# Optimization experiments

Measured on AMD Instinct MI355X. Metric: run time of the kernel, lower is better.

The kernel has to match this reference:

```python
import math
import jax, jax.numpy as jnp
import numpy as np

HEAD = 16
DIM = 1024
DH = DIM // HEAD
NEG = -100000000.0


def setup_inputs() -> dict:
    key = jax.random.key(0)
    ks = jax.random.split(key, 12)
    B, S, D = 2, 2048, DIM
    s = 1.0 / math.sqrt(D)
    return {
        "key": jax.random.normal(ks[0], (B, S, D), jnp.float32),
        "value": jax.random.normal(ks[1], (B, S, D), jnp.float32),
        "query": jax.random.normal(ks[2], (B, S, D), jnp.float32),
        "mask": jax.random.randint(ks[3], (B, 1, S, S), 0, 2) == 1,
        "Wq": jax.random.normal(ks[4], (D, D), jnp.float32) * s,
        "bq": jnp.zeros((D,), jnp.float32),
        "Wk": jax.random.normal(ks[5], (D, D), jnp.float32) * s,
        "bk": jnp.zeros((D,), jnp.float32),
        "Wv": jax.random.normal(ks[6], (D, D), jnp.float32) * s,
        "bv": jnp.zeros((D,), jnp.float32),
        "Wo": jax.random.normal(ks[7], (D, D), jnp.float32) * s,
        "bo": jnp.zeros((D,), jnp.float32),
    }


def _split_heads(x, b):
    # [B, S, D] -> [B, H, S, Dh]
    return x.reshape(b, -1, HEAD, DH).transpose(0, 2, 1, 3)


def reference(key, value, query, mask, Wq, bq, Wk, bk, Wv, bv, Wo, bo):
    b, k_len, d = key.shape
    q_len = query.shape[1]
    k_up = _split_heads(key @ Wk.T + bk, b)
    v_up = _split_heads(value @ Wv.T + bv, b)
    q_up = _split_heads(query @ Wq.T + bq, b) / math.sqrt(DH)
    scores = jnp.einsum("bhqd,bhkd->bhqk", q_up, k_up)
    scores = jnp.where(mask, NEG, scores)
    attn = jax.nn.softmax(scores, axis=-1)
    # dropout is identity in eval/reference mode
    context = jnp.einsum("bhqk,bhkd->bhqd", attn, v_up)
    context = context.transpose(0, 2, 1, 3).reshape(b, q_len, d)
    out = context @ Wo.T + bo
    return out, attn
```

## Files before the change

### kernel.cpp

```cpp
#include <hip/hip_runtime.h>
#include <stdint.h>

#define S_LEN 2048
#define D_MODEL 1024
#define N_HEAD 16
#define D_HEAD 64
#define N_BATCH 2
#define M_TOK (N_BATCH * S_LEN)

typedef unsigned short u16;
typedef unsigned int u32;
typedef __attribute__((ext_vector_type(8))) short bf16x8;
typedef __attribute__((ext_vector_type(4))) short s16x4;
typedef __attribute__((ext_vector_type(4))) float f32x4;
typedef __attribute__((ext_vector_type(4))) unsigned short u16x4;

#define MFMA16(a, b, c) __builtin_amdgcn_mfma_f32_16x16x32_bf16((a), (b), (c), 0, 0, 0)

#if defined(__has_builtin)
#if __has_builtin(__builtin_amdgcn_mfma_f32_16x16x16bf16_1k)
#define HAVE_MFMA_16x16x16 1
#define MFMA_PV(a, b, c) __builtin_amdgcn_mfma_f32_16x16x16bf16_1k((a), (b), (c), 0, 0, 0)
#endif
#endif

#define WAITCNT(n) asm volatile("s_waitcnt vmcnt(" #n ")" ::: "memory")
#define BAR() __builtin_amdgcn_s_barrier()

__device__ __forceinline__ u16 f2bf(float f) {
  unsigned int u = __float_as_uint(f);
  u = (u + 0x7FFFu + ((u >> 16) & 1u)) >> 16;
  return (u16)u;
}

__device__ __forceinline__ void gload_lds16(const u16* g, u16* l) {
  __builtin_amdgcn_global_load_lds((const __attribute__((address_space(1))) void*)g,
                                   (__attribute__((address_space(3))) void*)l, 16, 0, 0);
}

#define N4BIG (M_TOK * D_MODEL / 4)
#define N4W (D_MODEL * D_MODEL / 4)
__global__ __launch_bounds__(256) void cvt7_kernel(
    const float* __restrict__ sk, const float* __restrict__ sv, const float* __restrict__ sq,
    const float* __restrict__ swq, const float* __restrict__ swk, const float* __restrict__ swv,
    const float* __restrict__ swo, u16* __restrict__ dk, u16* __restrict__ dv, u16* __restrict__ dq,
    u16* __restrict__ dwq, u16* __restrict__ dwk, u16* __restrict__ dwv, u16* __restrict__ dwo) {
  const float* s;
  u16* d;
  int n4;
  switch (blockIdx.y) {
    case 0: s = sk; d = dk; n4 = N4BIG; break;
    case 1: s = sv; d = dv; n4 = N4BIG; break;
    case 2: s = sq; d = dq; n4 = N4BIG; break;
    case 3: s = swq; d = dwq; n4 = N4W; break;
    case 4: s = swk; d = dwk; n4 = N4W; break;
    case 5: s = swv; d = dwv; n4 = N4W; break;
    default: s = swo; d = dwo; n4 = N4W; break;
  }
  int i = blockIdx.x * blockDim.x + threadIdx.x;
  int stride = gridDim.x * blockDim.x;
  for (; i < n4; i += stride) {
    float4 v = ((const float4*)s)[i];
    u16x4 o = {f2bf(v.x), f2bf(v.y), f2bf(v.z), f2bf(v.w)};
    ((u16x4*)d)[i] = o;
  }
}

__global__ __launch_bounds__(256) void pack_mask(const int* __restrict__ mask,
                                                 unsigned long long* __restrict__ packed) {
  int wid = (blockIdx.x * blockDim.x + threadIdx.x) >> 6;
  int lane = threadIdx.x & 63;
  int nw = (gridDim.x * blockDim.x) >> 6;
  const int NW64 = M_TOK * (S_LEN / 64);
  for (int widx = wid; widx < NW64; widx += nw) {
    int m = mask[(size_t)widx * 64 + lane];
    unsigned long long bits = __ballot(m != 0);
    if (lane == 0) packed[widx] = bits;
  }
}

__device__ __forceinline__ void gemm_body(const u16* __restrict__ A, const u16* __restrict__ Bw,
                                          const float* __restrict__ bias, void* __restrict__ Cout,
                                          float scale, int outmode) {
  __shared__ u16 As[128 * 32];
  __shared__ u16 Bs[128 * 32];
  const int K = D_MODEL, N = D_MODEL;
  int tid = threadIdx.x;
  int w = tid >> 6, lane = tid & 63, lg = lane >> 4, lr = lane & 15;
  int m0 = blockIdx.x * 128, n0 = blockIdx.y * 128;
  int wr = w >> 1, wc = w & 1;
  f32x4 acc[4][4] = {};
  int r0 = tid >> 2;
  int r1 = 64 + (tid >> 2);
  int kk0 = (tid & 3) * 8;
  for (int kb = 0; kb < K; kb += 32) {
    gload_lds16(A + (size_t)(m0 + r0) * K + kb + kk0, As + w * 512);
    gload_lds16(A + (size_t)(m0 + r1) * K + kb + kk0, As + 2048 + w * 512);
    gload_lds16(Bw + (size_t)(n0 + r0) * K + kb + kk0, Bs + w * 512);
    gload_lds16(Bw + (size_t)(n0 + r1) * K + kb + kk0, Bs + 2048 + w * 512);
    __syncthreads();
    bf16x8 af[4], bfr[4];
#pragma unroll
    for (int i = 0; i < 4; i++)
      af[i] = *(const bf16x8*)(As + (wr * 64 + i * 16 + lr) * 32 + lg * 8);
#pragma unroll
    for (int i = 0; i < 4; i++)
      bfr[i] = *(const bf16x8*)(Bs + (wc * 64 + i * 16 + lr) * 32 + lg * 8);
#pragma unroll
    for (int mi = 0; mi < 4; mi++)
#pragma unroll
      for (int ni = 0; ni < 4; ni++)
        acc[mi][ni] = MFMA16(af[mi], bfr[ni], acc[mi][ni]);
    __syncthreads();
  }
#pragma unroll
  for (int mi = 0; mi < 4; mi++)
#pragma unroll
    for (int ni = 0; ni < 4; ni++) {
      int col = n0 + wc * 64 + ni * 16 + lr;
      float bv = bias[col];
      if (outmode == 2) {
        int row0 = m0 + wr * 64 + mi * 16 + lg * 4;
        int bb = row0 >> 11, ss = row0 & (S_LEN - 1);
        u16x4 pk;
#pragma unroll
        for (int r = 0; r < 4; r++) pk[r] = f2bf((acc[mi][ni][r] + bv) * scale);
        *(u16x4*)((u16*)Cout + ((size_t)((bb * N_HEAD + (col >> 6)) * D_HEAD + (col & 63)) * S_LEN + ss)) = pk;
      } else {
#pragma unroll
        for (int r = 0; r < 4; r++) {
          int row = m0 + wr * 64 + mi * 16 + lg * 4 + r;
          float v = (acc[mi][ni][r] + bv) * scale;
          if (outmode == 1)
            ((float*)Cout)[(size_t)row * N + col] = v;
          else
            ((u16*)Cout)[(size_t)row * N + col] = f2bf(v);
        }
      }
    }
}

#define QSCALE 0.18033688011112042f

__global__ __launch_bounds__(256) void proj3_kernel(
    const u16* __restrict__ kbf, const u16* __restrict__ vbf, const u16* __restrict__ qbf,
    const u16* __restrict__ wkb, const u16* __restrict__ wvb, const u16* __restrict__ wqb,
    const float* __restrict__ bk, const float* __restrict__ bv, const float* __restrict__ bq,
    u16* __restrict__ kup, u16* __restrict__ vtg, u16* __restrict__ qup) {
  int z = blockIdx.z;
  if (z == 0)
    gemm_body(kbf, wkb, bk, kup, 1.0f, 0);
  else if (z == 1)
    gemm_body(vbf, wvb, bv, vtg, 1.0f, 2);
  else
    gemm_body(qbf, wqb, bq, qup, QSCALE, 0);
}

__global__ __launch_bounds__(256) void gemm_out_kernel(const u16* __restrict__ A,
                                                       const u16* __restrict__ Bw,
                                                       const float* __restrict__ bias,
                                                       float* __restrict__ C) {
  gemm_body(A, Bw, bias, C, 1.0f, 1);
}

__global__ __launch_bounds__(512, 4) void attn_kernel(
    const u16* __restrict__ Qup, const u16* __restrict__ Kup, const u16* __restrict__ Vt,
    const u32* __restrict__ mpack, float* __restrict__ attn_out, u16* __restrict__ ctx) {
  __shared__ u16 kbuf[2][128 * 64];
  __shared__ u16 vbuf[2][64 * 128];
#if !defined(HAVE_MFMA_16x16x16)
  __shared__ u16 pbuf[8][16 * 64];
#endif
  int tid = threadIdx.x;
  int w = tid >> 6, lane = tid & 63, lg = lane >> 4, lr = lane & 15;

  int fb = blockIdx.x;
  int logical = (fb & 7) * 64 + (fb >> 3);
  int qx = logical & 15;
  int h = (logical >> 4) & 15;
  int b = logical >> 8;
  int q0 = qx * 128;
  int q = q0 + w * 16 + lr;
  const float NEGV = -100000000.0f;

  bf16x8 qf0, qf1;
  {
    const u16* qrow = Qup + (size_t)(b * S_LEN + q) * D_MODEL + h * D_HEAD;
    qf0 = *(const bf16x8*)(qrow + lg * 8);
    qf1 = *(const bf16x8*)(qrow + 32 + lg * 8);
  }
  const u16* Kb = Kup + (size_t)(b * S_LEN) * D_MODEL + h * D_HEAD;
  const u16* Vb = Vt + (size_t)(b * N_HEAD + h) * D_HEAD * S_LEN;
  const u32* mrow = mpack + (size_t)(b * S_LEN + q) * (S_LEN / 32);
  float* attn_b = attn_out + ((size_t)(b * N_HEAD + h) * S_LEN + q) * S_LEN;

  int krow = tid >> 3;
  int kchunk = (tid & 7) ^ (krow & 7);
  const u16* KgA = Kb + (size_t)krow * D_MODEL + kchunk * 8;
  int vrow = tid >> 4;
  int vchunk = (tid & 15) ^ (vrow & 7);
  const u16* VgA = Vb + (size_t)vrow * S_LEN + vchunk * 8;
  const int sw = lr & 7;

#define STAGE_K(bn, ktn)                                                    \
  do {                                                                      \
    const u16* _s = KgA + (size_t)(ktn) * 128 * D_MODEL;                    \
    gload_lds16(_s, &kbuf[bn][0] + w * 512);                                \
    gload_lds16(_s + (size_t)64 * D_MODEL, &kbuf[bn][4096] + w * 512);      \
  } while (0)
#define STAGE_V(bn, ktn)                                                    \
  do {                                                                      \
    const u16* _s = VgA + (size_t)(ktn) * 128;                              \
    gload_lds16(_s, &vbuf[bn][0] + w * 512);                                \
    gload_lds16(_s + (size_t)32 * S_LEN, &vbuf[bn][4096] + w * 512);        \
  } while (0)

  float lsA = 0.f, lsB = 0.f;

#define P0_BODY(BN, MM)                                                     \
  {                                                                         \
    const u16* kc = &kbuf[BN][0];                                           \
    _Pragma("unroll") for (int t = 0; t < 8; t++) {                         \
      const u16* kr = kc + (t * 16 + lr) * 64;                              \
      bf16x8 k0 = *(const bf16x8*)(kr + ((lg ^ sw) << 3));                  \
      bf16x8 k1 = *(const bf16x8*)(kr + (((lg + 4) ^ sw) << 3));            \
      f32x4 a = {0.f, 0.f, 0.f, 0.f};                                       \
      a = MFMA16(k0, qf0, a);                                               \
      a = MFMA16(k1, qf1, a);                                               \
      u32 wbits = (t >> 1) == 0 ? (MM).x                                    \
                : (t >> 1) == 1 ? (MM).y                                    \
                : (t >> 1) == 2 ? (MM).z : (MM).w;                          \
      _Pragma("unroll") for (int r = 0; r < 4; r++) {                       \
        int j = (t * 16 + lg * 4 + r) & 31;                                 \
        float s = ((wbits >> j) & 1u) ? NEGV : a[r];                        \
        if (r & 1) lsB += exp2f(s); else lsA += exp2f(s);                   \
      }                                                                     \
    }                                                                       \
  }

  uint4 mA, mB;
  mA = *(const uint4*)(mrow);
  STAGE_K(0, 0);
  for (int it = 0; it < 7; it++) {
    int kt = it * 2;
    mB = *(const uint4*)(mrow + (kt + 1) * 4);
    STAGE_K(1, kt + 1);
    WAITCNT(3);
    BAR();
    P0_BODY(0, mA);
    BAR();
    mA = *(const uint4*)(mrow + (kt + 2) * 4);
    STAGE_K(0, kt + 2);
    WAITCNT(3);
    BAR();
    P0_BODY(1, mB);
    BAR();
  }
  mB = *(const uint4*)(mrow + 15 * 4);
  STAGE_K(1, 15);
  WAITCNT(3);
  BAR();
  P0_BODY(0, mA);
  BAR();
  WAITCNT(0);
  BAR();
  P0_BODY(1, mB);

  float lsum = lsA + lsB;
  lsum += __shfl_xor(lsum, 16);
  lsum += __shfl_xor(lsum, 32);
  float il2 = lsum > 0.f ? -__log2f(lsum) : 0.f;

  BAR();

  f32x4 ctxacc[4] = {};

#if defined(HAVE_MFMA_16x16x16)
#define P1_BODY(BN, MM, KT)                                                 \
  {                                                                         \
    const u16* kc = &kbuf[BN][0];                                           \
    const u16* vc = &vbuf[BN][0];                                           \
    _Pragma("unroll") for (int t = 0; t < 8; t++) {                         \
      const u16* kr = kc + (t * 16 + lr) * 64;                              \
      bf16x8 k0 = *(const bf16x8*)(kr + ((lg ^ sw) << 3));                  \
      bf16x8 k1 = *(const bf16x8*)(kr + (((lg + 4) ^ sw) << 3));            \
      f32x4 a = {0.f, 0.f, 0.f, 0.f};                                       \
      a = MFMA16(k0, qf0, a);                                                \
      a = MFMA16(k1, qf1, a);                                                \
      u32 wbits = (t >> 1) == 0 ? (MM).x                                    \
                : (t >> 1) == 1 ? (MM).y                                    \
                : (t >> 1) == 2 ? (MM).z : (MM).w;                          \
      f32x4 p;                                                              \
      u16x4 pb;                                                             \
      _Pragma("unroll") for (int r = 0; r < 4; r++) {                       \
        int j = (t * 16 + lg * 4 + r) & 31;                                 \
        float s = ((wbits >> j) & 1u) ? NEGV : (a[r] + il2);                \
        float pv = exp2f(s);                                                \
        p[r] = pv;                                                          \
        pb[r] = f2bf(pv);                                                   \
      }                                                                     \
      *(f32x4*)(attn_b + (KT) * 128 + t * 16 + lg * 4) = p;                 \
      s16x4 ap = {(short)pb[0], (short)pb[1], (short)pb[2], (short)pb[3]};  \
      _Pragma("unroll") for (int d = 0; d < 4; d++) {                       \
        s16x4 vf = *(const s16x4*)(vc + (d * 16 + lr) * 128 +               \
                                   (((t * 2 + (lg >> 1)) ^ sw) << 3) +      \
                                   ((lg & 1) << 2));                        \
        ctxacc[d] = MFMA_PV(ap, vf, ctxacc[d]);                             \
      }                                                                     \
    }                                                                       \
  }
#else
#define P1_BODY(BN, MM, KT)                                                 \
  {                                                                         \
    const u16* kc = &kbuf[BN][0];                                           \
    const u16* vc = &vbuf[BN][0];                                           \
    u16* pw = &pbuf[w][0];                                                  \
    _Pragma("unroll") for (int h2 = 0; h2 < 2; h2++) {                      \
      _Pragma("unroll") for (int tt = 0; tt < 4; tt++) {                    \
        const int t = h2 * 4 + tt;                                          \
        const u16* kr = kc + (t * 16 + lr) * 64;                            \
        bf16x8 k0 = *(const bf16x8*)(kr + ((lg ^ sw) << 3));                \
        bf16x8 k1 = *(const bf16x8*)(kr + (((lg + 4) ^ sw) << 3));          \
        f32x4 a = {0.f, 0.f, 0.f, 0.f};                                     \
        a = MFMA16(k0, qf0, a);                                              \
        a = MFMA16(k1, qf1, a);                                              \
        u32 wbits = (t >> 1) == 0 ? (MM).x                                  \
                  : (t >> 1) == 1 ? (MM).y                                  \
                  : (t >> 1) == 2 ? (MM).z : (MM).w;                        \
        f32x4 p;                                                            \
        u16x4 pb;                                                           \
        _Pragma("unroll") for (int r = 0; r < 4; r++) {                     \
          int j = (t * 16 + lg * 4 + r) & 31;                               \
          float s = ((wbits >> j) & 1u) ? NEGV : (a[r] + il2);              \
          float pv = exp2f(s);                                              \
          p[r] = pv;                                                        \
          pb[r] = f2bf(pv);                                                 \
        }                                                                   \
        *(f32x4*)(attn_b + (KT) * 128 + t * 16 + lg * 4) = p;               \
        *(u16x4*)(pw + lr * 64 + (((tt * 2 + (lg >> 1)) ^ sw) << 3) +       \
                  ((lg & 1) << 2)) = pb;                                    \
      }                                                                     \
      bf16x8 pa0 = *(const bf16x8*)(pw + lr * 64 + ((lg ^ sw) << 3));       \
      bf16x8 pa1 = *(const bf16x8*)(pw + lr * 64 + (((lg + 4) ^ sw) << 3)); \
      _Pragma("unroll") for (int d = 0; d < 4; d++) {                       \
        const u16* vr = vc + (d * 16 + lr) * 128 + (h2 << 6);               \
        bf16x8 v0 = *(const bf16x8*)(vr + ((lg ^ sw) << 3));                \
        bf16x8 v1 = *(const bf16x8*)(vr + (((lg + 4) ^ sw) << 3));          \
        ctxacc[d] = MFMA16(pa0, v0, ctxacc[d]);                             \
        ctxacc[d] = MFMA16(pa1, v1, ctxacc[d]);                             \
      }                                                                     \
    }                                                                       \
  }
#endif

  mA = *(const uint4*)(mrow);
  STAGE_K(0, 0);
  STAGE_V(0, 0);
  for (int it = 0; it < 7; it++) {
    int kt = it * 2;
    mB = *(const uint4*)(mrow + (kt + 1) * 4);
    STAGE_K(1, kt + 1);
    STAGE_V(1, kt + 1);
    WAITCNT(5);
    BAR();
    P1_BODY(0, mA, kt);
    BAR();
    mA = *(const uint4*)(mrow + (kt + 2) * 4);
    STAGE_K(0, kt + 2);
    STAGE_V(0, kt + 2);
    WAITCNT(5);
    BAR();
    P1_BODY(1, mB, kt + 1);
    BAR();
  }
  mB = *(const uint4*)(mrow + 15 * 4);
  STAGE_K(1, 15);
  STAGE_V(1, 15);
  WAITCNT(5);
  BAR();
  P1_BODY(0, mA, 14);
  BAR();
  WAITCNT(8);
  BAR();
  P1_BODY(1, mB, 15);

#pragma unroll
  for (int d = 0; d < 4; d++)
#pragma unroll
    for (int r = 0; r < 4; r++) {
      int sq = q0 + w * 16 + lg * 4 + r;
      ctx[(size_t)(b * S_LEN + sq) * D_MODEL + h * D_HEAD + d * 16 + lr] = f2bf(ctxacc[d][r]);
    }
#undef STAGE_K
#undef STAGE_V
#undef P0_BODY
#undef P1_BODY
}

#define O_KBF 0u
#define O_VBF 4194304u
#define O_QBF 8388608u
#define O_WQ 12582912u
#define O_WK 13631488u
#define O_WV 14680064u
#define O_WO 15728640u
#define O_QUP 16777216u
#define O_KUP 20971520u
#define O_VUP 25165824u
#define O_CTX 29360128u

extern "C" void kernel_launch(void* const* d_in, const int* in_sizes, int n_in,
                              void* d_out, int out_size, void* d_ws, size_t ws_size,
                              hipStream_t stream) {
  const float* key = (const float*)d_in[0];
  const float* value = (const float*)d_in[1];
  const float* query = (const float*)d_in[2];
  const int* mask = (const int*)d_in[3];
  const float* Wq = (const float*)d_in[4];
  const float* bq = (const float*)d_in[5];
  const float* Wk = (const float*)d_in[6];
  const float* bk = (const float*)d_in[7];
  const float* Wv = (const float*)d_in[8];
  const float* bv = (const float*)d_in[9];
  const float* Wo = (const float*)d_in[10];
  const float* bo = (const float*)d_in[11];

  u16* ws = (u16*)d_ws;
  u16* kbf = ws + O_KBF;
  u16* vbf = ws + O_VBF;
  u16* qbf = ws + O_QBF;
  u16* wqb = ws + O_WQ;
  u16* wkb = ws + O_WK;
  u16* wvb = ws + O_WV;
  u16* wob = ws + O_WO;
  u16* qup = ws + O_QUP;
  u16* kup = ws + O_KUP;
  u16* vtg = ws + O_VUP;
  u16* ctxb = ws + O_CTX;

  float* out = (float*)d_out;
  float* attn = out + (size_t)N_BATCH * S_LEN * D_MODEL;

  cvt7_kernel<<<dim3(512, 7), 256, 0, stream>>>(key, value, query, Wq, Wk, Wv, Wo, kbf, vbf, qbf,
                                                wqb, wkb, wvb, wob);
  proj3_kernel<<<dim3(32, 8, 3), 256, 0, stream>>>(kbf, vbf, qbf, wkb, wvb, wqb, bk, bv, bq, kup,
                                                   vtg, qup);
  pack_mask<<<1024, 256, 0, stream>>>(mask, (unsigned long long*)kbf);
  attn_kernel<<<512, 512, 0, stream>>>(qup, kup, vtg, (const u32*)kbf, attn, ctxb);
  gemm_out_kernel<<<dim3(32, 8), 256, 0, stream>>>(ctxb, wob, bo, out);
}
```

Baseline: 330.6 us.

## Load V fragments straight from global and use a 4-deep K LDS ring

The V tile is no longer staged through shared memory. Each wave reads its V operand fragments directly from global memory inside the PV loop. The LDS freed by dropping V is used for a 4-buffer ring of K tiles, staged two tiles ahead, which removes one barrier per tile in both passes. This cuts LDS traffic and synchronisation, but the direct V reads are small 8-byte, strided global loads that may add latency and waste bandwidth unless they hit cache.

```diff
diff --git a/kernel.cpp b/kernel.cpp
--- a/kernel.cpp
+++ b/kernel.cpp
@@ -166,8 +166,7 @@
 __global__ __launch_bounds__(512, 4) void attn_kernel(
     const u16* __restrict__ Qup, const u16* __restrict__ Kup, const u16* __restrict__ Vt,
     const u32* __restrict__ mpack, float* __restrict__ attn_out, u16* __restrict__ ctx) {
-  __shared__ u16 kbuf[2][128 * 64];
-  __shared__ u16 vbuf[2][64 * 128];
+  __shared__ u16 kbuf[4][128 * 64];
 #if !defined(HAVE_MFMA_16x16x16)
   __shared__ u16 pbuf[8][16 * 64];
 #endif
@@ -197,9 +196,6 @@
   int krow = tid >> 3;
   int kchunk = (tid & 7) ^ (krow & 7);
   const u16* KgA = Kb + (size_t)krow * D_MODEL + kchunk * 8;
-  int vrow = tid >> 4;
-  int vchunk = (tid & 15) ^ (vrow & 7);
-  const u16* VgA = Vb + (size_t)vrow * S_LEN + vchunk * 8;
   const int sw = lr & 7;
 
 #define STAGE_K(bn, ktn)                                                    \
@@ -207,12 +203,6 @@
     const u16* _s = KgA + (size_t)(ktn) * 128 * D_MODEL;                    \
     gload_lds16(_s, &kbuf[bn][0] + w * 512);                                \
     gload_lds16(_s + (size_t)64 * D_MODEL, &kbuf[bn][4096] + w * 512);      \
-  } while (0)
-#define STAGE_V(bn, ktn)                                                    \
-  do {                                                                      \
-    const u16* _s = VgA + (size_t)(ktn) * 128;                              \
-    gload_lds16(_s, &vbuf[bn][0] + w * 512);                                \
-    gload_lds16(_s + (size_t)32 * S_LEN, &vbuf[bn][4096] + w * 512);        \
   } while (0)
 
   float lsA = 0.f, lsB = 0.f;
@@ -241,30 +231,27 @@
   uint4 mA, mB;
   mA = *(const uint4*)(mrow);
   STAGE_K(0, 0);
+  STAGE_K(1, 1);
   for (int it = 0; it < 7; it++) {
     int kt = it * 2;
     mB = *(const uint4*)(mrow + (kt + 1) * 4);
-    STAGE_K(1, kt + 1);
-    WAITCNT(3);
+    STAGE_K((kt + 2) & 3, kt + 2);
+    WAITCNT(5);
     BAR();
-    P0_BODY(0, mA);
+    P0_BODY(kt & 3, mA);
+    mA = *(const uint4*)(mrow + (kt + 2) * 4);
+    STAGE_K((kt + 3) & 3, kt + 3);
+    WAITCNT(5);
     BAR();
-    mA = *(const uint4*)(mrow + (kt + 2) * 4);
-    STAGE_K(0, kt + 2);
-    WAITCNT(3);
-    BAR();
-    P0_BODY(1, mB);
-    BAR();
+    P0_BODY((kt + 1) & 3, mB);
   }
   mB = *(const uint4*)(mrow + 15 * 4);
-  STAGE_K(1, 15);
   WAITCNT(3);
   BAR();
-  P0_BODY(0, mA);
-  BAR();
+  P0_BODY(2, mA);
   WAITCNT(0);
   BAR();
-  P0_BODY(1, mB);
+  P0_BODY(3, mB);
 
   float lsum = lsA + lsB;
   lsum += __shfl_xor(lsum, 16);
@@ -279,14 +266,18 @@
 #define P1_BODY(BN, MM, KT)                                                 \
   {                                                                         \
     const u16* kc = &kbuf[BN][0];                                           \
-    const u16* vc = &vbuf[BN][0];                                           \
+    const u16* vg = Vb + (size_t)(KT) * 128;                                \
     _Pragma("unroll") for (int t = 0; t < 8; t++) {                         \
+      s16x4 vf0 = *(const s16x4*)(vg + (size_t)(0 * 16 + lr) * S_LEN + t * 16 + lg * 4); \
+      s16x4 vf1 = *(const s16x4*)(vg + (size_t)(1 * 16 + lr) * S_LEN + t * 16 + lg * 4); \
+      s16x4 vf2 = *(const s16x4*)(vg + (size_t)(2 * 16 + lr) * S_LEN + t * 16 + lg * 4); \
+      s16x4 vf3 = *(const s16x4*)(vg + (size_t)(3 * 16 + lr) * S_LEN + t * 16 + lg * 4); \
       const u16* kr = kc + (t * 16 + lr) * 64;                              \
       bf16x8 k0 = *(const bf16x8*)(kr + ((lg ^ sw) << 3));                  \
       bf16x8 k1 = *(const bf16x8*)(kr + (((lg + 4) ^ sw) << 3));            \
       f32x4 a = {0.f, 0.f, 0.f, 0.f};                                       \
-      a = MFMA16(k0, qf0, a);                                                \
-      a = MFMA16(k1, qf1, a);                                                \
+      a = MFMA16(k0, qf0, a);                                               \
+      a = MFMA16(k1, qf1, a);                                               \
       u32 wbits = (t >> 1) == 0 ? (MM).x                                    \
                 : (t >> 1) == 1 ? (MM).y                                    \
                 : (t >> 1) == 2 ? (MM).z : (MM).w;                          \
@@ -301,19 +292,17 @@
       }                                                                     \
       *(f32x4*)(attn_b + (KT) * 128 + t * 16 + lg * 4) = p;                 \
       s16x4 ap = {(short)pb[0], (short)pb[1], (short)pb[2], (short)pb[3]};  \
-      _Pragma("unroll") for (int d = 0; d < 4; d++) {                       \
-        s16x4 vf = *(const s16x4*)(vc + (d * 16 + lr) * 128 +               \
-                                   (((t * 2 + (lg >> 1)) ^ sw) << 3) +      \
-                                   ((lg & 1) << 2));                        \
-        ctxacc[d] = MFMA_PV(ap, vf, ctxacc[d]);                             \
-      }                                                                     \
+      ctxacc[0] = MFMA_PV(ap, vf0, ctxacc[0]);                              \
+      ctxacc[1] = MFMA_PV(ap, vf1, ctxacc[1]);                              \
+      ctxacc[2] = MFMA_PV(ap, vf2, ctxacc[2]);                              \
+      ctxacc[3] = MFMA_PV(ap, vf3, ctxacc[3]);                              \
     }                                                                       \
   }
 #else
 #define P1_BODY(BN, MM, KT)                                                 \
   {                                                                         \
     const u16* kc = &kbuf[BN][0];                                           \
-    const u16* vc = &vbuf[BN][0];                                           \
+    const u16* vg = Vb + (size_t)(KT) * 128;                                \
     u16* pw = &pbuf[w][0];                                                  \
     _Pragma("unroll") for (int h2 = 0; h2 < 2; h2++) {                      \
       _Pragma("unroll") for (int tt = 0; tt < 4; tt++) {                    \
@@ -343,9 +332,9 @@
       bf16x8 pa0 = *(const bf16x8*)(pw + lr * 64 + ((lg ^ sw) << 3));       \
       bf16x8 pa1 = *(const bf16x8*)(pw + lr * 64 + (((lg + 4) ^ sw) << 3)); \
       _Pragma("unroll") for (int d = 0; d < 4; d++) {                       \
-        const u16* vr = vc + (d * 16 + lr) * 128 + (h2 << 6);               \
-        bf16x8 v0 = *(const bf16x8*)(vr + ((lg ^ sw) << 3));                \
-        bf16x8 v1 = *(const bf16x8*)(vr + (((lg + 4) ^ sw) << 3));          \
+        const u16* vr = vg + (size_t)(d * 16 + lr) * S_LEN + h2 * 64;       \
+        bf16x8 v0 = *(const bf16x8*)(vr + lg * 8);                          \
+        bf16x8 v1 = *(const bf16x8*)(vr + 32 + lg * 8);                     \
         ctxacc[d] = MFMA16(pa0, v0, ctxacc[d]);                             \
         ctxacc[d] = MFMA16(pa1, v1, ctxacc[d]);                             \
       }                                                                     \
@@ -355,34 +344,27 @@
 
   mA = *(const uint4*)(mrow);
   STAGE_K(0, 0);
-  STAGE_V(0, 0);
+  STAGE_K(1, 1);
   for (int it = 0; it < 7; it++) {
     int kt = it * 2;
     mB = *(const uint4*)(mrow + (kt + 1) * 4);
-    STAGE_K(1, kt + 1);
-    STAGE_V(1, kt + 1);
+    STAGE_K((kt + 2) & 3, kt + 2);
     WAITCNT(5);
     BAR();
-    P1_BODY(0, mA, kt);
-    BAR();
+    P1_BODY(kt & 3, mA, kt);
     mA = *(const uint4*)(mrow + (kt + 2) * 4);
-    STAGE_K(0, kt + 2);
-    STAGE_V(0, kt + 2);
+    STAGE_K((kt + 3) & 3, kt + 3);
     WAITCNT(5);
     BAR();
-    P1_BODY(1, mB, kt + 1);
-    BAR();
+    P1_BODY((kt + 1) & 3, mB, kt + 1);
   }
   mB = *(const uint4*)(mrow + 15 * 4);
-  STAGE_K(1, 15);
-  STAGE_V(1, 15);
-  WAITCNT(5);
+  WAITCNT(3);
   BAR();
-  P1_BODY(0, mA, 14);
+  P1_BODY(2, mA, 14);
+  WAITCNT(0);
   BAR();
-  WAITCNT(8);
-  BAR();
-  P1_BODY(1, mB, 15);
+  P1_BODY(3, mB, 15);
 
 #pragma unroll
   for (int d = 0; d < 4; d++)
@@ -392,7 +374,6 @@
       ctx[(size_t)(b * S_LEN + sq) * D_MODEL + h * D_HEAD + d * 16 + lr] = f2bf(ctxacc[d][r]);
     }
 #undef STAGE_K
-#undef STAGE_V
 #undef P0_BODY
 #undef P1_BODY
 }
```

After: 468.7 us. 1.42x slower.

## Split attention into separate row-sum and probability/PV kernels with LDS-staged attn writes

Applied to the files above, without the earlier changes.

Splits the two-pass attention kernel into two launches. The first computes softmax row sums over half of the keys per block, using 2048 smaller blocks for more parallelism, and writes partial sums to workspace. The second kernel reads the two partial sums, uses 64-key tiles instead of 128, and stages each wave's fp32 probabilities through padded LDS so the attn matrix is written as coalesced row segments. The cost is an extra launch, extra K reads and mask reads in the first pass, more LDS use, and more barrier iterations.

```diff
diff --git a/kernel.cpp b/kernel.cpp
--- a/kernel.cpp
+++ b/kernel.cpp
@@ -163,17 +163,109 @@
   gemm_body(A, Bw, bias, C, 1.0f, 1);
 }
 
-__global__ __launch_bounds__(512, 4) void attn_kernel(
-    const u16* __restrict__ Qup, const u16* __restrict__ Kup, const u16* __restrict__ Vt,
-    const u32* __restrict__ mpack, float* __restrict__ attn_out, u16* __restrict__ ctx) {
-  __shared__ u16 kbuf[2][128 * 64];
-  __shared__ u16 vbuf[2][64 * 128];
-#if !defined(HAVE_MFMA_16x16x16)
-  __shared__ u16 pbuf[8][16 * 64];
-#endif
+__global__ __launch_bounds__(256, 8) void attn_p0(const u16* __restrict__ Qup,
+                                                  const u16* __restrict__ Kup,
+                                                  const u32* __restrict__ mpack,
+                                                  float* __restrict__ lsums) {
+  __shared__ u16 kbuf[2][64 * 64];
   int tid = threadIdx.x;
   int w = tid >> 6, lane = tid & 63, lg = lane >> 4, lr = lane & 15;
-
+  int fb = blockIdx.x;
+  int logical = (fb & 7) * 256 + (fb >> 3);
+  int khalf = logical & 1;
+  int qb = (logical >> 1) & 31;
+  int h = (logical >> 6) & 15;
+  int b = logical >> 10;
+  int q0 = qb * 64;
+  int q = q0 + w * 16 + lr;
+  const float NEGV = -100000000.0f;
+
+  bf16x8 qf0, qf1;
+  {
+    const u16* qrow = Qup + (size_t)(b * S_LEN + q) * D_MODEL + h * D_HEAD;
+    qf0 = *(const bf16x8*)(qrow + lg * 8);
+    qf1 = *(const bf16x8*)(qrow + 32 + lg * 8);
+  }
+  const u16* Kb = Kup + (size_t)(b * S_LEN) * D_MODEL + h * D_HEAD;
+  const u32* mrow = mpack + (size_t)(b * S_LEN + q) * (S_LEN / 32) + khalf * 32;
+
+  int srow = tid >> 3;
+  int schunk = (tid & 7) ^ (srow & 7);
+  const u16* KgA = Kb + (size_t)(khalf * 1024 + srow) * D_MODEL + schunk * 8;
+  const int sw = lr & 7;
+
+#define STAGE_K0(bn, ktn)                                                   \
+  do {                                                                      \
+    const u16* _s = KgA + (size_t)(ktn) * 64 * D_MODEL;                     \
+    gload_lds16(_s, &kbuf[bn][0] + w * 512);                                \
+    gload_lds16(_s + (size_t)32 * D_MODEL, &kbuf[bn][2048] + w * 512);      \
+  } while (0)
+
+  float lsA = 0.f, lsB = 0.f;
+#define P0_BODY(BN, MM)                                                     \
+  {                                                                         \
+    const u16* kc = &kbuf[BN][0];                                           \
+    _Pragma("unroll") for (int t = 0; t < 4; t++) {                         \
+      const u16* kr = kc + (t * 16 + lr) * 64;                              \
+      bf16x8 k0 = *(const bf16x8*)(kr + ((lg ^ sw) << 3));                  \
+      bf16x8 k1 = *(const bf16x8*)(kr + (((lg + 4) ^ sw) << 3));            \
+      f32x4 a = {0.f, 0.f, 0.f, 0.f};                                       \
+      a = MFMA16(k0, qf0, a);                                               \
+      a = MFMA16(k1, qf1, a);                                               \
+      u32 wbits = (t < 2) ? (MM).x : (MM).y;                                \
+      _Pragma("unroll") for (int r = 0; r < 4; r++) {                       \
+        int j = (t * 16 + lg * 4 + r) & 31;                                 \
+        float s = ((wbits >> j) & 1u) ? NEGV : a[r];                        \
+        if (r & 1) lsB += exp2f(s); else lsA += exp2f(s);                   \
+      }                                                                     \
+    }                                                                       \
+  }
+
+  uint2 mA, mB;
+  mA = *(const uint2*)(mrow);
+  STAGE_K0(0, 0);
+  for (int it = 0; it < 7; it++) {
+    int kt = it * 2;
+    mB = *(const uint2*)(mrow + (kt + 1) * 2);
+    STAGE_K0(1, kt + 1);
+    WAITCNT(3);
+    BAR();
+    P0_BODY(0, mA);
+    BAR();
+    mA = *(const uint2*)(mrow + (kt + 2) * 2);
+    STAGE_K0(0, kt + 2);
+    WAITCNT(3);
+    BAR();
+    P0_BODY(1, mB);
+    BAR();
+  }
+  mB = *(const uint2*)(mrow + 15 * 2);
+  STAGE_K0(1, 15);
+  WAITCNT(3);
+  BAR();
+  P0_BODY(0, mA);
+  BAR();
+  WAITCNT(0);
+  BAR();
+  P0_BODY(1, mB);
+
+  float lsum = lsA + lsB;
+  lsum += __shfl_xor(lsum, 16);
+  lsum += __shfl_xor(lsum, 32);
+  if (lg == 0) lsums[(size_t)khalf * 65536 + (size_t)(b * N_HEAD + h) * S_LEN + q] = lsum;
+#undef STAGE_K0
+#undef P0_BODY
+}
+
+__global__ __launch_bounds__(512, 4) void attn_p1(
+    const u16* __restrict__ Qup, const u16* __restrict__ Kup, const u16* __restrict__ Vt,
+    const u32* __restrict__ mpack, const float* __restrict__ lsums,
+    float* __restrict__ attn_out, u16* __restrict__ ctx) {
+  __shared__ u16 kbuf[2][64 * 64];
+  __shared__ u16 vbuf[2][64 * 64];
+  __shared__ float pbuf[8][16][68];
+  int tid = threadIdx.x;
+  int w = tid >> 6, lane = tid & 63, lg = lane >> 4, lr = lane & 15;
   int fb = blockIdx.x;
   int logical = (fb & 7) * 64 + (fb >> 3);
   int qx = logical & 15;
@@ -192,104 +284,54 @@
   const u16* Kb = Kup + (size_t)(b * S_LEN) * D_MODEL + h * D_HEAD;
   const u16* Vb = Vt + (size_t)(b * N_HEAD + h) * D_HEAD * S_LEN;
   const u32* mrow = mpack + (size_t)(b * S_LEN + q) * (S_LEN / 32);
-  float* attn_b = attn_out + ((size_t)(b * N_HEAD + h) * S_LEN + q) * S_LEN;
-
-  int krow = tid >> 3;
-  int kchunk = (tid & 7) ^ (krow & 7);
-  const u16* KgA = Kb + (size_t)krow * D_MODEL + kchunk * 8;
-  int vrow = tid >> 4;
-  int vchunk = (tid & 15) ^ (vrow & 7);
-  const u16* VgA = Vb + (size_t)vrow * S_LEN + vchunk * 8;
+  float* attn_w = attn_out + ((size_t)(b * N_HEAD + h) * S_LEN + q0 + w * 16) * S_LEN;
+
+  float il2;
+  {
+    size_t idx = (size_t)(b * N_HEAD + h) * S_LEN + q;
+    float tot = lsums[idx] + lsums[65536 + idx];
+    il2 = tot > 0.f ? -__log2f(tot) : 0.f;
+  }
+
+  int srow = tid >> 3;
+  int schunk = (tid & 7) ^ (srow & 7);
+  const u16* KgA = Kb + (size_t)srow * D_MODEL + schunk * 8;
+  const u16* VgA = Vb + (size_t)srow * S_LEN + schunk * 8;
   const int sw = lr & 7;
 
-#define STAGE_K(bn, ktn)                                                    \
-  do {                                                                      \
-    const u16* _s = KgA + (size_t)(ktn) * 128 * D_MODEL;                    \
-    gload_lds16(_s, &kbuf[bn][0] + w * 512);                                \
-    gload_lds16(_s + (size_t)64 * D_MODEL, &kbuf[bn][4096] + w * 512);      \
-  } while (0)
-#define STAGE_V(bn, ktn)                                                    \
-  do {                                                                      \
-    const u16* _s = VgA + (size_t)(ktn) * 128;                              \
-    gload_lds16(_s, &vbuf[bn][0] + w * 512);                                \
-    gload_lds16(_s + (size_t)32 * S_LEN, &vbuf[bn][4096] + w * 512);        \
-  } while (0)
-
-  float lsA = 0.f, lsB = 0.f;
-
-#define P0_BODY(BN, MM)                                                     \
+#define SK(bn, ktn) gload_lds16(KgA + (size_t)(ktn) * 64 * D_MODEL, &kbuf[bn][w * 512])
+#define SV(bn, ktn) gload_lds16(VgA + (size_t)(ktn) * 64, &vbuf[bn][w * 512])
+
+  f32x4 ctxacc[4] = {};
+
+#if defined(HAVE_MFMA_16x16x16)
+#define PV_STEP(vc, t)                                                      \
+  {                                                                         \
+    s16x4 ap = {(short)pb[0], (short)pb[1], (short)pb[2], (short)pb[3]};    \
+    _Pragma("unroll") for (int d = 0; d < 4; d++) {                         \
+      s16x4 vf = *(const s16x4*)((vc) + (d * 16 + lr) * 64 +                \
+                                 ((((t)*2 + (lg >> 1)) ^ sw) << 3) +        \
+                                 ((lg & 1) << 2));                          \
+      ctxacc[d] = MFMA_PV(ap, vf, ctxacc[d]);                               \
+    }                                                                       \
+  }
+#else
+#define PV_STEP(vc, t) (void)pb;
+#endif
+
+#define P1_BODY(BN, MM, KT)                                                 \
   {                                                                         \
     const u16* kc = &kbuf[BN][0];                                           \
-    _Pragma("unroll") for (int t = 0; t < 8; t++) {                         \
+    const u16* vc = &vbuf[BN][0];                                           \
+    float* pw = &pbuf[w][0][0];                                             \
+    _Pragma("unroll") for (int t = 0; t < 4; t++) {                         \
       const u16* kr = kc + (t * 16 + lr) * 64;                              \
       bf16x8 k0 = *(const bf16x8*)(kr + ((lg ^ sw) << 3));                  \
       bf16x8 k1 = *(const bf16x8*)(kr + (((lg + 4) ^ sw) << 3));            \
       f32x4 a = {0.f, 0.f, 0.f, 0.f};                                       \
       a = MFMA16(k0, qf0, a);                                               \
       a = MFMA16(k1, qf1, a);                                               \
-      u32 wbits = (t >> 1) == 0 ? (MM).x                                    \
-                : (t >> 1) == 1 ? (MM).y                                    \
-                : (t >> 1) == 2 ? (MM).z : (MM).w;                          \
-      _Pragma("unroll") for (int r = 0; r < 4; r++) {                       \
-        int j = (t * 16 + lg * 4 + r) & 31;                                 \
-        float s = ((wbits >> j) & 1u) ? NEGV : a[r];                        \
-        if (r & 1) lsB += exp2f(s); else lsA += exp2f(s);                   \
-      }                                                                     \
-    }                                                                       \
-  }
-
-  uint4 mA, mB;
-  mA = *(const uint4*)(mrow);
-  STAGE_K(0, 0);
-  for (int it = 0; it < 7; it++) {
-    int kt = it * 2;
-    mB = *(const uint4*)(mrow + (kt + 1) * 4);
-    STAGE_K(1, kt + 1);
-    WAITCNT(3);
-    BAR();
-    P0_BODY(0, mA);
-    BAR();
-    mA = *(const uint4*)(mrow + (kt + 2) * 4);
-    STAGE_K(0, kt + 2);
-    WAITCNT(3);
-    BAR();
-    P0_BODY(1, mB);
-    BAR();
-  }
-  mB = *(const uint4*)(mrow + 15 * 4);
-  STAGE_K(1, 15);
-  WAITCNT(3);
-  BAR();
-  P0_BODY(0, mA);
-  BAR();
-  WAITCNT(0);
-  BAR();
-  P0_BODY(1, mB);
-
-  float lsum = lsA + lsB;
-  lsum += __shfl_xor(lsum, 16);
-  lsum += __shfl_xor(lsum, 32);
-  float il2 = lsum > 0.f ? -__log2f(lsum) : 0.f;
-
-  BAR();
-
-  f32x4 ctxacc[4] = {};
-
-#if defined(HAVE_MFMA_16x16x16)
-#define P1_BODY(BN, MM, KT)                                                 \
-  {                                                                         \
-    const u16* kc = &kbuf[BN][0];                                           \
-    const u16* vc = &vbuf[BN][0];                                           \
-    _Pragma("unroll") for (int t = 0; t < 8; t++) {                         \
-      const u16* kr = kc + (t * 16 + lr) * 64;                              \
-      bf16x8 k0 = *(const bf16x8*)(kr + ((lg ^ sw) << 3));                  \
-      bf16x8 k1 = *(const bf16x8*)(kr + (((lg + 4) ^ sw) << 3));            \
-      f32x4 a = {0.f, 0.f, 0.f, 0.f};                                       \
-      a = MFMA16(k0, qf0, a);                                                \
-      a = MFMA16(k1, qf1, a);                                                \
-      u32 wbits = (t >> 1) == 0 ? (MM).x                                    \
-                : (t >> 1) == 1 ? (MM).y                                    \
-                : (t >> 1) == 2 ? (MM).z : (MM).w;                          \
+      u32 wbits = (t < 2) ? (MM).x : (MM).y;                                \
       f32x4 p;                                                              \
       u16x4 pb;                                                             \
       _Pragma("unroll") for (int r = 0; r < 4; r++) {                       \
@@ -299,90 +341,86 @@
         p[r] = pv;                                                          \
         pb[r] = f2bf(pv);                                                   \
       }                                                                     \
-      *(f32x4*)(attn_b + (KT) * 128 + t * 16 + lg * 4) = p;                 \
-      s16x4 ap = {(short)pb[0], (short)pb[1], (short)pb[2], (short)pb[3]};  \
-      _Pragma("unroll") for (int d = 0; d < 4; d++) {                       \
-        s16x4 vf = *(const s16x4*)(vc + (d * 16 + lr) * 128 +               \
-                                   (((t * 2 + (lg >> 1)) ^ sw) << 3) +      \
-                                   ((lg & 1) << 2));                        \
-        ctxacc[d] = MFMA_PV(ap, vf, ctxacc[d]);                             \
-      }                                                                     \
-    }                                                                       \
-  }
+      *(f32x4*)(pw + lr * 68 + t * 16 + lg * 4) = p;                        \
+      PV_STEP(vc, t)                                                        \
+    }                                                                       \
+                    \
+    P1_FALLBACK_PV(vc)                                                      \
+             \
+    _Pragma("unroll") for (int i = 0; i < 4; i++) {                         \
+      int rl = (lane >> 4) + i * 4;                                         \
+      int cc = lane & 15;                                                   \
+      f32x4 v = *(const f32x4*)(&pbuf[w][0][0] + rl * 68 + cc * 4);         \
+      *(f32x4*)(attn_w + (size_t)rl * S_LEN + (KT) * 64 + cc * 4) = v;      \
+    }                                                                       \
+  }
+
+#if defined(HAVE_MFMA_16x16x16)
+#define P1_FALLBACK_PV(vc)
 #else
-#define P1_BODY(BN, MM, KT)                                                 \
+#define P1_FALLBACK_PV(vc)                                                  \
   {                                                                         \
-    const u16* kc = &kbuf[BN][0];                                           \
-    const u16* vc = &vbuf[BN][0];                                           \
-    u16* pw = &pbuf[w][0];                                                  \
-    _Pragma("unroll") for (int h2 = 0; h2 < 2; h2++) {                      \
-      _Pragma("unroll") for (int tt = 0; tt < 4; tt++) {                    \
-        const int t = h2 * 4 + tt;                                          \
-        const u16* kr = kc + (t * 16 + lr) * 64;                            \
-        bf16x8 k0 = *(const bf16x8*)(kr + ((lg ^ sw) << 3));                \
-        bf16x8 k1 = *(const bf16x8*)(kr + (((lg + 4) ^ sw) << 3));          \
-        f32x4 a = {0.f, 0.f, 0.f, 0.f};                                     \
-        a = MFMA16(k0, qf0, a);                                              \
-        a = MFMA16(k1, qf1, a);                                              \
-        u32 wbits = (t >> 1) == 0 ? (MM).x                                  \
-                  : (t >> 1) == 1 ? (MM).y                                  \
-                  : (t >> 1) == 2 ? (MM).z : (MM).w;                        \
-        f32x4 p;                                                            \
-        u16x4 pb;                                                           \
-        _Pragma("unroll") for (int r = 0; r < 4; r++) {                     \
-          int j = (t * 16 + lg * 4 + r) & 31;                               \
-          float s = ((wbits >> j) & 1u) ? NEGV : (a[r] + il2);              \
-          float pv = exp2f(s);                                              \
-          p[r] = pv;                                                        \
-          pb[r] = f2bf(pv);                                                 \
-        }                                                                   \
-        *(f32x4*)(attn_b + (KT) * 128 + t * 16 + lg * 4) = p;               \
-        *(u16x4*)(pw + lr * 64 + (((tt * 2 + (lg >> 1)) ^ sw) << 3) +       \
-                  ((lg & 1) << 2)) = pb;                                    \
-      }                                                                     \
-      bf16x8 pa0 = *(const bf16x8*)(pw + lr * 64 + ((lg ^ sw) << 3));       \
-      bf16x8 pa1 = *(const bf16x8*)(pw + lr * 64 + (((lg + 4) ^ sw) << 3)); \
-      _Pragma("unroll") for (int d = 0; d < 4; d++) {                       \
-        const u16* vr = vc + (d * 16 + lr) * 128 + (h2 << 6);               \
-        bf16x8 v0 = *(const bf16x8*)(vr + ((lg ^ sw) << 3));                \
-        bf16x8 v1 = *(const bf16x8*)(vr + (((lg + 4) ^ sw) << 3));          \
-        ctxacc[d] = MFMA16(pa0, v0, ctxacc[d]);                             \
-        ctxacc[d] = MFMA16(pa1, v1, ctxacc[d]);                             \
-      }                                                                     \
+    float* pw = &pbuf[w][0][0];                                             \
+    bf16x8 pa0, pa1;                                                        \
+    _Pragma("unroll") for (int e = 0; e < 8; e++) {                         \
+      pa0[e] = (short)f2bf(pw[lr * 68 + lg * 8 + e]);                       \
+      pa1[e] = (short)f2bf(pw[lr * 68 + 32 + lg * 8 + e]);                  \
+    }                                                                       \
+    _Pragma("unroll") for (int d = 0; d < 4; d++) {                         \
+      const u16* vr = (vc) + (d * 16 + lr) * 64;                            \
+      bf16x8 v0 = *(const bf16x8*)(vr + ((lg ^ sw) << 3));                  \
+      bf16x8 v1 = *(const bf16x8*)(vr + (((lg + 4) ^ sw) << 3));            \
+      ctxacc[d] = MFMA16(pa0, v0, ctxacc[d]);                               \
+      ctxacc[d] = MFMA16(pa1, v1, ctxacc[d]);                               \
     }                                                                       \
   }
 #endif
 
-  mA = *(const uint4*)(mrow);
-  STAGE_K(0, 0);
-  STAGE_V(0, 0);
-  for (int it = 0; it < 7; it++) {
+  uint2 mA, mB;
+  mA = *(const uint2*)(mrow);
+  SK(0, 0);
+  SV(0, 0);
+  mB = *(const uint2*)(mrow + 1 * 2);
+  SK(1, 1);
+  SV(1, 1);
+  WAITCNT(3);
+  BAR();
+  P1_BODY(0, mA, 0);
+  BAR();
+  mA = *(const uint2*)(mrow + 2 * 2);
+  SK(0, 2);
+  SV(0, 2);
+  WAITCNT(7);
+  BAR();
+  P1_BODY(1, mB, 1);
+  BAR();
+  for (int it = 1; it < 15; it++) {
     int kt = it * 2;
-    mB = *(const uint4*)(mrow + (kt + 1) * 4);
-    STAGE_K(1, kt + 1);
-    STAGE_V(1, kt + 1);
-    WAITCNT(5);
+    mB = *(const uint2*)(mrow + (kt + 1) * 2);
+    SK(1, kt + 1);
+    SV(1, kt + 1);
+    WAITCNT(7);
     BAR();
     P1_BODY(0, mA, kt);
     BAR();
-    mA = *(const uint4*)(mrow + (kt + 2) * 4);
-    STAGE_K(0, kt + 2);
-    STAGE_V(0, kt + 2);
-    WAITCNT(5);
+    mA = *(const uint2*)(mrow + (kt + 2) * 2);
+    SK(0, kt + 2);
+    SV(0, kt + 2);
+    WAITCNT(7);
     BAR();
     P1_BODY(1, mB, kt + 1);
     BAR();
   }
-  mB = *(const uint4*)(mrow + 15 * 4);
-  STAGE_K(1, 15);
-  STAGE_V(1, 15);
-  WAITCNT(5);
-  BAR();
-  P1_BODY(0, mA, 14);
-  BAR();
-  WAITCNT(8);
-  BAR();
-  P1_BODY(1, mB, 15);
+  mB = *(const uint2*)(mrow + 31 * 2);
+  SK(1, 31);
+  SV(1, 31);
+  WAITCNT(7);
+  BAR();
+  P1_BODY(0, mA, 30);
+  BAR();
+  WAITCNT(4);
+  BAR();
+  P1_BODY(1, mB, 31);
 
 #pragma unroll
   for (int d = 0; d < 4; d++)
@@ -391,10 +429,11 @@
       int sq = q0 + w * 16 + lg * 4 + r;
       ctx[(size_t)(b * S_LEN + sq) * D_MODEL + h * D_HEAD + d * 16 + lr] = f2bf(ctxacc[d][r]);
     }
-#undef STAGE_K
-#undef STAGE_V
-#undef P0_BODY
+#undef SK
+#undef SV
 #undef P1_BODY
+#undef PV_STEP
+#undef P1_FALLBACK_PV
 }
 
 #define O_KBF 0u
@@ -437,6 +476,7 @@
   u16* kup = ws + O_KUP;
   u16* vtg = ws + O_VUP;
   u16* ctxb = ws + O_CTX;
+  float* lsums = (float*)(ws + O_VBF);
 
   float* out = (float*)d_out;
   float* attn = out + (size_t)N_BATCH * S_LEN * D_MODEL;
@@ -446,6 +486,7 @@
   proj3_kernel<<<dim3(32, 8, 3), 256, 0, stream>>>(kbf, vbf, qbf, wkb, wvb, wqb, bk, bv, bq, kup,
                                                    vtg, qup);
   pack_mask<<<1024, 256, 0, stream>>>(mask, (unsigned long long*)kbf);
-  attn_kernel<<<512, 512, 0, stream>>>(qup, kup, vtg, (const u32*)kbf, attn, ctxb);
+  attn_p0<<<2048, 256, 0, stream>>>(qup, kup, (const u32*)kbf, lsums);
+  attn_p1<<<512, 512, 0, stream>>>(qup, kup, vtg, (const u32*)kbf, lsums, attn, ctxb);
   gemm_out_kernel<<<dim3(32, 8), 256, 0, stream>>>(ctxb, wob, bo, out);
 }
```

New measurement: 333.8 us. About the same (+1.0%).
